# Kernel tuning notes

Measured on AMD Instinct MI355X. Metric: run time of the kernel, lower is better.

The kernel has to match this reference:

```python
import jax, jax.numpy as jnp
import numpy as np

T, D_IN, H, E = 8192, 2048, 2048, 512


def setup_inputs() -> dict:
    key = jax.random.key(0)
    k_x, k_wi, k_wh, k_wo = jax.random.split(key, 4)
    s_in = 1.0 / np.sqrt(D_IN)
    s_h = 1.0 / np.sqrt(H)
    return {
        "inputs": jax.random.normal(k_x, (T, D_IN), dtype=jnp.float32),
        "w_i": jax.random.normal(k_wi, (D_IN, 3 * H), dtype=jnp.float32) * s_in,
        "w_h": jax.random.normal(k_wh, (H, 3 * H), dtype=jnp.float32) * s_h,
        "b": jnp.zeros((3 * H,), dtype=jnp.float32),
        "w_out": jax.random.normal(k_wo, (H, E), dtype=jnp.float32) * s_h,
        "b_out": jnp.zeros((E,), dtype=jnp.float32),
    }


def reference(inputs, w_i, w_h, b, w_out, b_out):
    h_size = w_h.shape[0]
    w_h_zr = w_h[:, : 2 * h_size]   # [H, 2H]
    w_h_a = w_h[:, 2 * h_size :]    # [H, H]
    b_zr = b[: 2 * h_size]
    b_a = b[2 * h_size :]

    def step(h, x):
        gates_x = x @ w_i                       # [3H]
        zr_x = gates_x[: 2 * h_size]
        a_x = gates_x[2 * h_size :]
        zr = jax.nn.sigmoid(zr_x + h @ w_h_zr + b_zr)
        z, r = zr[:h_size], zr[h_size:]
        a = jnp.tanh(a_x + (r * h) @ w_h_a + b_a)
        h_new = (1.0 - z) * h + z * a
        return h_new, None

    h0 = jnp.zeros((h_size,), dtype=inputs.dtype)
    h_final, _ = jax.lax.scan(step, h0, inputs)
    return h_final @ w_out + b_out
```

## Files before the change

### kernel.cpp

```cpp
#include <hip/hip_runtime.h>
#include <stdint.h>

#define T_STEPS 8192
#define DIN     2048
#define HD      2048
#define G3      6144
#define EOUT    512

#define NA 64
#define NB 64
#define HP 1024
#define NREP 8
#define SPIN_MAX (1<<20)

typedef unsigned long long u64;
typedef __attribute__((ext_vector_type(8))) __bf16 bf16x8;
typedef __attribute__((ext_vector_type(8))) unsigned short u16x8;
typedef __attribute__((ext_vector_type(4))) float f32x4;

__device__ __forceinline__ uint16_t f2bf(float v){
  uint32_t x = __float_as_uint(v);
  return (uint16_t)((x + 0x7fffu + ((x >> 16) & 1u)) >> 16);
}

__device__ __forceinline__ u64 aload(const u64* p){
  return __hip_atomic_load(p, __ATOMIC_RELAXED, __HIP_MEMORY_SCOPE_AGENT);
}
__device__ __forceinline__ void astore(u64* p, u64 v){
  __hip_atomic_store(p, v, __ATOMIC_RELAXED, __HIP_MEMORY_SCOPE_AGENT);
}

__device__ __forceinline__ bf16x8 load_afrag(const float* __restrict__ w, int col, int kb){
  u16x8 r;
  #pragma unroll
  for (int j = 0; j < 8; ++j)
    r[j] = f2bf(w[(size_t)(kb + j)*G3 + col]);
  return __builtin_bit_cast(bf16x8, r);
}

template<bool OWN>
__device__ __forceinline__ u64 poll_slice(const u64* src, uint32_t want,
                                          uint32_t* lds_slice, int own_base,
                                          int lane, volatile int* deadp){
  const u64* p0 = src + 2*lane;
  const u64* p1 = p0 + 1;
  const u64* po = src + own_base + lane;
  const bool need_own = OWN && (lane < 16);
  u64 v0, v1, vo = 0;
  int spins = 0;
  for(;;){
    v0 = aload(p0); v1 = aload(p1);
    if (need_own) vo = aload(po);
    bool ok = (uint32_t)(v0 >> 32) >= want && (uint32_t)(v1 >> 32) >= want &&
              (!need_own || (uint32_t)(vo >> 32) >= want);
    if (__all(ok)) break;
    if ((++spins & 63) == 0){
      if (*deadp) break;
      if (spins > SPIN_MAX){ *deadp = 1; break; }
    }
    __builtin_amdgcn_s_sleep(1);
  }
  u64 pk = ((u64)(uint32_t)v1 << 32) | (u64)(uint32_t)v0;
  *(u64*)&lds_slice[2*lane] = pk;
  return vo;
}

__device__ __forceinline__ void mv_pass(const uint32_t* vp,
                                        const bf16x8* wA, const bf16x8* wB,
                                        float* red, int wid, int lane){
  const int boff = (lane >> 4) << 2;
  f32x4 acc0 = {0.f,0.f,0.f,0.f}, acc1 = {0.f,0.f,0.f,0.f};
  #pragma unroll
  for (int s = 0; s < 8; ++s){
    uint4 bu = *(const uint4*)(vp + s*16 + boff);
    bf16x8 bf = __builtin_bit_cast(bf16x8, bu);
    acc0 = __builtin_amdgcn_mfma_f32_16x16x32_bf16(wA[s], bf, acc0, 0, 0, 0);
    acc1 = __builtin_amdgcn_mfma_f32_16x16x32_bf16(wB[s], bf, acc1, 0, 0, 0);
  }
  if ((lane & 15) == 0){
    int mb = (lane >> 4) << 2;
    #pragma unroll
    for (int r = 0; r < 4; ++r){
      red[(mb + r)*9 + wid]      = acc0[r];
      red[(16 + mb + r)*9 + wid] = acc1[r];
    }
  }
}

__global__ __launch_bounds__(512) void gates_gemm(const float* __restrict__ A,
                                                  const float* __restrict__ B,
                                                  float* __restrict__ C){
  __shared__ uint16_t Asb[128*40];
  __shared__ uint16_t Bsb[128*40];
  const int bm = blockIdx.x / (G3/128);
  const int bn = blockIdx.x % (G3/128);
  const int row0 = bm*128, col0 = bn*128;
  const int tid  = threadIdx.x;
  const int lane = tid & 63, wid = tid >> 6;
  const int wr = wid >> 2, wc = wid & 3;
  f32x4 acc[4][2] = {};
  for (int k0 = 0; k0 < DIN; k0 += 32){
    {
      int m = tid >> 2, ks = (tid & 3) * 8;
      const float* src = A + (size_t)(row0 + m)*DIN + k0 + ks;
      float4 f0 = *(const float4*)src;
      float4 f1 = *(const float4*)(src + 4);
      u16x8 pk;
      pk[0]=f2bf(f0.x); pk[1]=f2bf(f0.y); pk[2]=f2bf(f0.z); pk[3]=f2bf(f0.w);
      pk[4]=f2bf(f1.x); pk[5]=f2bf(f1.y); pk[6]=f2bf(f1.z); pk[7]=f2bf(f1.w);
      *(u16x8*)(Asb + m*40 + ks) = pk;
    }
    {
      int k = tid >> 4, n8 = tid & 15;
      const float* src = B + (size_t)(k0 + k)*G3 + col0 + n8;
      #pragma unroll
      for (int i = 0; i < 8; ++i)
        Bsb[(n8 + 16*i)*40 + k] = f2bf(src[16*i]);
    }
    __syncthreads();
    const int mrow = wr*64, ncol = wc*32;
    const int fm = lane & 15, fk = (lane >> 4) * 8;
    bf16x8 bfr[2];
    #pragma unroll
    for (int j = 0; j < 2; ++j)
      bfr[j] = *(const bf16x8*)(Bsb + (ncol + j*16 + fm)*40 + fk);
    #pragma unroll
    for (int i = 0; i < 4; ++i){
      bf16x8 af = *(const bf16x8*)(Asb + (mrow + i*16 + fm)*40 + fk);
      acc[i][0] = __builtin_amdgcn_mfma_f32_16x16x32_bf16(af, bfr[0], acc[i][0], 0,0,0);
      acc[i][1] = __builtin_amdgcn_mfma_f32_16x16x32_bf16(af, bfr[1], acc[i][1], 0,0,0);
    }
    __syncthreads();
  }
  const int mrow = row0 + wr*64, ncol = col0 + wc*32;
  #pragma unroll
  for (int i = 0; i < 4; ++i)
    #pragma unroll
    for (int j = 0; j < 2; ++j){
      int cc = ncol + j*16 + (lane & 15);
      int rr = mrow + i*16 + (lane >> 4)*4;
      #pragma unroll
      for (int q = 0; q < 4; ++q)
        C[(size_t)(rr + q)*G3 + cc] = acc[i][j][q];
    }
}

__global__ __launch_bounds__(512) void scan_kernel(
    const float* __restrict__ gates, const float* __restrict__ w_h,
    const float* __restrict__ b,
    u64* hbuf, u64* rhbuf, float* hfinal)
{
  __shared__ uint32_t vph[2][1024];
  __shared__ uint32_t vprh[2][1024];
  __shared__ float    red0[32*9];
  __shared__ float    red1[32*9];
  __shared__ float    gx[2][64];
  __shared__ float    hloc[2][32];
  __shared__ int      dead;
  volatile int* deadp = &dead;

  const int tid  = threadIdx.x;
  const int lane = tid & 63;
  const int wid  = tid >> 6;
  const bool isA = blockIdx.x < NA;
  const int  g   = isA ? (int)blockIdx.x : (int)blockIdx.x - NA;
  const int  rep = blockIdx.x & (NREP - 1);

  bf16x8 w0[8], w1[8], w2[8], w3[8];
  {
    const int kb0 = wid*256 + ((lane >> 4) << 3);
    const int c0  = isA ? (2048 + 32*g) : (32*g);
    #pragma unroll
    for (int s = 0; s < 8; ++s){
      w0[s] = load_afrag(w_h, c0 + (lane & 15),      kb0 + s*32);
      w1[s] = load_afrag(w_h, c0 + 16 + (lane & 15), kb0 + s*32);
    }
    if (!isA){
      const int ca = 4096 + 32*g;
      #pragma unroll
      for (int s = 0; s < 8; ++s){
        w2[s] = load_afrag(w_h, ca + (lane & 15),      kb0 + s*32);
        w3[s] = load_afrag(w_h, ca + 16 + (lane & 15), kb0 + s*32);
      }
    }
  }

  if (tid == 0) *deadp = 0;
  if (tid < 64) ((float*)hloc)[tid] = 0.f;

  int   gcol = -1;
  float bias = 0.f;
  if (isA) { if (tid < 32) gcol = 2048 + 32*g + tid; }
  else     { if (tid < 32)      gcol = 32*g + tid;
             else if (tid < 64) gcol = 4096 + 32*g + (tid - 32);}
  if (gcol >= 0) { bias = b[gcol]; gx[0][tid] = gates[gcol] + bias; }
  __syncthreads();

  for (int t = 0; t < T_STEPS; ++t){
    const int par = t & 1;

    if (isA){
      const u64* src = hbuf + ((size_t)(rep*2 + par))*HP;
      u64 vo;
      if (wid == 0)
        vo = poll_slice<true >(src, (uint32_t)t, &vph[par][0],       16*g, lane, deadp);
      else
        vo = poll_slice<false>(src + wid*128, (uint32_t)t,
                               &vph[par][wid*128], 0, lane, deadp);
      mv_pass(&vph[par][wid*128], w0, w1, red0, wid, lane);
      __syncthreads();
      if (*deadp) break;
      if (wid == 0){
        uint32_t hp = __shfl((int)(uint32_t)vo, lane >> 1);
        if (lane < 32){
          float acc = 0.f;
          #pragma unroll
          for (int w = 0; w < 8; ++w) acc += red0[lane*9 + w];
          float pre = acc + gx[par][lane];
          float r = 1.f / (1.f + __expf(-pre));
          float hval = __uint_as_float((lane & 1) ? (hp & 0xffff0000u) : (hp << 16));
          float rh = r * hval;
          float other = __shfl_xor(rh, 1);
          if (!(lane & 1)){
            u64 pv = ((u64)(uint32_t)(t + 1) << 32)
                   | ((u64)f2bf(other) << 16) | (u64)f2bf(rh);
            size_t idx = (size_t)((32*g + lane) >> 1);
            #pragma unroll
            for (int rp = 0; rp < NREP; ++rp)
              astore(rhbuf + (size_t)(rp*2 + par)*HP + idx, pv);
          }
          int tn = (t + 1 < T_STEPS) ? t + 1 : t;
          gx[par ^ 1][lane] = gates[(size_t)tn*G3 + gcol] + bias;
        }
      }
    } else {
      const u64* hsrc = hbuf + ((size_t)(rep*2 + par))*HP;
      poll_slice<false>(hsrc + wid*128, (uint32_t)t, &vph[par][wid*128], 0, lane, deadp);
      mv_pass(&vph[par][wid*128], w0, w1, red0, wid, lane);
      const u64* rsrc = rhbuf + ((size_t)(rep*2 + par))*HP;
      poll_slice<false>(rsrc + wid*128, (uint32_t)(t + 1), &vprh[par][wid*128], 0, lane, deadp);
      mv_pass(&vprh[par][wid*128], w2, w3, red1, wid, lane);
      __syncthreads();
      if (*deadp) break;
      if (wid == 0 && lane < 32){
        float zacc = 0.f, aacc = 0.f;
        #pragma unroll
        for (int w = 0; w < 8; ++w){ zacc += red0[lane*9 + w]; aacc += red1[lane*9 + w]; }
        float z = 1.f / (1.f + __expf(-(zacc + gx[par][lane])));
        float apre = aacc + gx[par][32 + lane];
        float e = __expf(2.f*apre);
        float a = 1.f - 2.f/(1.f + e);
        float hold = hloc[par][lane];
        float hnew = hold + z*(a - hold);
        hloc[par ^ 1][lane] = hnew;
        float other = __shfl_xor(hnew, 1);
        if (!(lane & 1)){
          u64 pv = ((u64)(uint32_t)(t + 1) << 32)
                 | ((u64)f2bf(other) << 16) | (u64)f2bf(hnew);
          size_t idx = (size_t)((32*g + lane) >> 1);
          #pragma unroll
          for (int rp = 0; rp < NREP; ++rp)
            astore(hbuf + (size_t)(rp*2 + ((t+1)&1))*HP + idx, pv);
        }
      }
      if (wid == 0 && gcol >= 0){
        int tn = (t + 1 < T_STEPS) ? t + 1 : t;
        gx[par ^ 1][lane] = gates[(size_t)tn*G3 + gcol] + bias;
      }
    }
  }

  if (!isA && tid < 32) hfinal[32*g + tid] = hloc[0][tid];
}

__global__ __launch_bounds__(1024) void out_proj(const float* __restrict__ hfin,
                                                 const float* __restrict__ w_out,
                                                 const float* __restrict__ b_out,
                                                 float* __restrict__ out){
  __shared__ float red[16][80];
  const int g  = blockIdx.x;
  const int cl = threadIdx.x & 63;
  const int kc = threadIdx.x >> 6;
  const int col = 64*g + cl;
  float acc = 0.f;
  for (int k = kc*128; k < kc*128 + 128; ++k)
    acc = fmaf(hfin[k], w_out[(size_t)k*EOUT + col], acc);
  red[kc][cl] = acc;
  __syncthreads();
  if (kc == 0){
    float s = 0.f;
    #pragma unroll
    for (int q = 0; q < 16; ++q) s += red[q][cl];
    out[col] = s + b_out[col];
  }
}

extern "C" void kernel_launch(void* const* d_in, const int* in_sizes, int n_in,
                              void* d_out, int out_size, void* d_ws, size_t ws_size,
                              hipStream_t stream) {
  const float* x     = (const float*)d_in[0];
  const float* w_i   = (const float*)d_in[1];
  const float* w_h   = (const float*)d_in[2];
  const float* b     = (const float*)d_in[3];
  const float* w_out = (const float*)d_in[4];
  const float* b_out = (const float*)d_in[5];
  float* out = (float*)d_out;

  float* gates  = (float*)d_ws;
  u64*   hbuf   = (u64*)(gates + (size_t)T_STEPS * G3);
  u64*   rhbuf  = hbuf + (size_t)NREP*2*HP;
  float* hfinal = (float*)(rhbuf + (size_t)NREP*2*HP);
  (void)in_sizes; (void)n_in; (void)out_size; (void)ws_size;

  hipMemsetAsync(hbuf, 0, (size_t)(2*NREP*2*HP)*sizeof(u64), stream);

  gates_gemm<<<dim3((T_STEPS/128)*(G3/128)), dim3(512), 0, stream>>>(x, w_i, gates);

  const float* gates_c = gates;
  void* kargs[6];
  kargs[0] = (void*)&gates_c;
  kargs[1] = (void*)&w_h;
  kargs[2] = (void*)&b;
  kargs[3] = (void*)&hbuf;
  kargs[4] = (void*)&rhbuf;
  kargs[5] = (void*)&hfinal;
  hipLaunchCooperativeKernel((void*)scan_kernel, dim3(NA + NB), dim3(512), kargs, 0u, stream);

  out_proj<<<dim3(EOUT/64), dim3(1024), 0, stream>>>(hfinal, w_out, b_out, out);
}
```

Baseline: 27.59 ms.

## Pipeline spin-poll loads and spread replica publishes across all waves

The polling loop now issues the next round of atomic loads before checking the previous round, so load latency overlaps the check. It also sleeps only every fourth spin and checks the dead flag less often. Each of the 8 waves now redundantly computes the gate epilogue and writes one replica slot, rather than wave 0 writing all NREP replicas serially. All waves also poll the own-slice values. This shortens the serial publish path on the recurrent critical path, at the cost of more redundant ALU work and memory polling traffic.

```diff
diff --git a/kernel.cpp b/kernel.cpp
--- a/kernel.cpp
+++ b/kernel.cpp
@@ -39,30 +39,32 @@
 }
 
 template<bool OWN>
-__device__ __forceinline__ u64 poll_slice(const u64* src, uint32_t want,
-                                          uint32_t* lds_slice, int own_base,
+__device__ __forceinline__ u64 poll_slice(const u64* slice, const u64* own_p,
+                                          uint32_t want, uint32_t* lds_slice,
                                           int lane, volatile int* deadp){
-  const u64* p0 = src + 2*lane;
+  const u64* p0 = slice + 2*lane;
   const u64* p1 = p0 + 1;
-  const u64* po = src + own_base + lane;
   const bool need_own = OWN && (lane < 16);
-  u64 v0, v1, vo = 0;
+  u64 a0 = aload(p0), a1 = aload(p1);
+  u64 ao = need_own ? aload(own_p) : 0;
   int spins = 0;
   for(;;){
-    v0 = aload(p0); v1 = aload(p1);
-    if (need_own) vo = aload(po);
-    bool ok = (uint32_t)(v0 >> 32) >= want && (uint32_t)(v1 >> 32) >= want &&
-              (!need_own || (uint32_t)(vo >> 32) >= want);
+    u64 b0 = aload(p0), b1 = aload(p1);
+    u64 bo = need_own ? aload(own_p) : 0;
+    bool ok = (uint32_t)(a0 >> 32) >= want &&
+              (uint32_t)(a1 >> 32) >= want &&
+              (!need_own || (uint32_t)(ao >> 32) >= want);
     if (__all(ok)) break;
-    if ((++spins & 63) == 0){
+    a0 = b0; a1 = b1; ao = bo;
+    ++spins;
+    if ((spins & 3) == 0) __builtin_amdgcn_s_sleep(1);
+    if ((spins & 255) == 0){
       if (*deadp) break;
       if (spins > SPIN_MAX){ *deadp = 1; break; }
     }
-    __builtin_amdgcn_s_sleep(1);
-  }
-  u64 pk = ((u64)(uint32_t)v1 << 32) | (u64)(uint32_t)v0;
-  *(u64*)&lds_slice[2*lane] = pk;
-  return vo;
+  }
+  *(u64*)&lds_slice[2*lane] = ((u64)(uint32_t)a1 << 32) | (u64)(uint32_t)a0;
+  return ao;
 }
 
 __device__ __forceinline__ void mv_pass(const uint32_t* vp,
@@ -201,48 +203,43 @@
 
     if (isA){
       const u64* src = hbuf + ((size_t)(rep*2 + par))*HP;
-      u64 vo;
-      if (wid == 0)
-        vo = poll_slice<true >(src, (uint32_t)t, &vph[par][0],       16*g, lane, deadp);
-      else
-        vo = poll_slice<false>(src + wid*128, (uint32_t)t,
-                               &vph[par][wid*128], 0, lane, deadp);
+      u64 vo = poll_slice<true>(src + wid*128, src + 16*g + lane, (uint32_t)t,
+                                &vph[par][wid*128], lane, deadp);
       mv_pass(&vph[par][wid*128], w0, w1, red0, wid, lane);
       __syncthreads();
       if (*deadp) break;
-      if (wid == 0){
-        uint32_t hp = __shfl((int)(uint32_t)vo, lane >> 1);
-        if (lane < 32){
-          float acc = 0.f;
-          #pragma unroll
-          for (int w = 0; w < 8; ++w) acc += red0[lane*9 + w];
-          float pre = acc + gx[par][lane];
-          float r = 1.f / (1.f + __expf(-pre));
-          float hval = __uint_as_float((lane & 1) ? (hp & 0xffff0000u) : (hp << 16));
-          float rh = r * hval;
-          float other = __shfl_xor(rh, 1);
-          if (!(lane & 1)){
-            u64 pv = ((u64)(uint32_t)(t + 1) << 32)
-                   | ((u64)f2bf(other) << 16) | (u64)f2bf(rh);
-            size_t idx = (size_t)((32*g + lane) >> 1);
-            #pragma unroll
-            for (int rp = 0; rp < NREP; ++rp)
-              astore(rhbuf + (size_t)(rp*2 + par)*HP + idx, pv);
-          }
+      uint32_t hp = __shfl((int)(uint32_t)vo, lane >> 1);
+      if (lane < 32){
+        float acc = 0.f;
+        #pragma unroll
+        for (int w = 0; w < 8; ++w) acc += red0[lane*9 + w];
+        float pre = acc + gx[par][lane];
+        float r = 1.f / (1.f + __expf(-pre));
+        float hval = __uint_as_float((lane & 1) ? (hp & 0xffff0000u) : (hp << 16));
+        float rh = r * hval;
+        float other = __shfl_xor(rh, 1);
+        if (!(lane & 1)){
+          u64 pv = ((u64)(uint32_t)(t + 1) << 32)
+                 | ((u64)f2bf(other) << 16) | (u64)f2bf(rh);
+          astore(rhbuf + (size_t)(wid*2 + par)*HP + (size_t)((32*g + lane) >> 1), pv);
+        }
+        if (wid == 0){
           int tn = (t + 1 < T_STEPS) ? t + 1 : t;
           gx[par ^ 1][lane] = gates[(size_t)tn*G3 + gcol] + bias;
         }
       }
     } else {
       const u64* hsrc = hbuf + ((size_t)(rep*2 + par))*HP;
-      poll_slice<false>(hsrc + wid*128, (uint32_t)t, &vph[par][wid*128], 0, lane, deadp);
+      poll_slice<false>(hsrc + wid*128, (const u64*)0, (uint32_t)t,
+                        &vph[par][wid*128], lane, deadp);
       mv_pass(&vph[par][wid*128], w0, w1, red0, wid, lane);
       const u64* rsrc = rhbuf + ((size_t)(rep*2 + par))*HP;
-      poll_slice<false>(rsrc + wid*128, (uint32_t)(t + 1), &vprh[par][wid*128], 0, lane, deadp);
+      poll_slice<false>(rsrc + wid*128, (const u64*)0, (uint32_t)(t + 1),
+                        &vprh[par][wid*128], lane, deadp);
       mv_pass(&vprh[par][wid*128], w2, w3, red1, wid, lane);
       __syncthreads();
       if (*deadp) break;
-      if (wid == 0 && lane < 32){
+      if (lane < 32){
         float zacc = 0.f, aacc = 0.f;
         #pragma unroll
         for (int w = 0; w < 8; ++w){ zacc += red0[lane*9 + w]; aacc += red1[lane*9 + w]; }
@@ -252,15 +249,12 @@
         float a = 1.f - 2.f/(1.f + e);
         float hold = hloc[par][lane];
         float hnew = hold + z*(a - hold);
-        hloc[par ^ 1][lane] = hnew;
+        if (wid == 0) hloc[par ^ 1][lane] = hnew;
         float other = __shfl_xor(hnew, 1);
         if (!(lane & 1)){
           u64 pv = ((u64)(uint32_t)(t + 1) << 32)
                  | ((u64)f2bf(other) << 16) | (u64)f2bf(hnew);
-          size_t idx = (size_t)((32*g + lane) >> 1);
-          #pragma unroll
-          for (int rp = 0; rp < NREP; ++rp)
-            astore(hbuf + (size_t)(rp*2 + ((t+1)&1))*HP + idx, pv);
+          astore(hbuf + (size_t)(wid*2 + ((t+1)&1))*HP + (size_t)((32*g + lane) >> 1), pv);
         }
       }
       if (wid == 0 && gcol >= 0){
```

Measured after the change: 30.76 ms. 11.5% more time.
